# Kernel tuning notes

Hardware: AMD Instinct MI355X
Metric: run time of the kernel (lower is better)

The kernel has to match this reference:

```python
import jax, jax.numpy as jnp
import numpy as np

H, FFN, E, TOPK = 1024, 4096, 8, 2
B, S = 2, 1024


def setup_inputs() -> dict:
    key = jax.random.key(0)
    k1, k2, k3, k4 = jax.random.split(key, 4)
    s_h = 1.0 / np.sqrt(H).astype(np.float32)
    s_f = 1.0 / np.sqrt(FFN).astype(np.float32)
    return {
        "hidden_states": jax.random.normal(k1, (B, S, H), jnp.float32),
        "gate_w": jax.random.normal(k2, (E, H), jnp.float32) * s_h,       # router Linear(H->E), no bias
        "w13": jax.random.normal(k3, (E, 2 * FFN, H), jnp.float32) * s_h,  # fused [w1; w3] per expert
        "w2": jax.random.normal(k4, (E, H, FFN), jnp.float32) * s_f,       # down-proj per expert
        "top_k": TOPK,
    }


def reference(hidden_states, gate_w, w13, w2, top_k):
    b, s, h = hidden_states.shape
    x = hidden_states.reshape(-1, h)                       # [T, H]
    router_logits = x @ gate_w.T                           # [T, E]
    rw = jax.nn.softmax(router_logits.astype(jnp.float32), axis=1)
    rw, sel = jax.lax.top_k(rw, top_k)                     # [T, K] each
    rw = rw / rw.sum(axis=-1, keepdims=True)
    rw = rw.astype(x.dtype)
    e_tot = gate_w.shape[0]
    f = w2.shape[2]
    # combine[t, e] = sum_k rw[t, k] * (sel[t, k] == e)
    combine = jnp.sum((sel[..., None] == jnp.arange(e_tot)) * rw[..., None], axis=1)  # [T, E]
    out = jnp.zeros_like(x)
    for e in range(e_tot):  # static small loop over experts
        g = x @ w13[e, :f].T            # [T, F] gate proj
        u = x @ w13[e, f:].T            # [T, F] up proj
        y = (jax.nn.silu(g) * u) @ w2[e].T  # [T, H]
        out = out + combine[:, e:e + 1] * y
    return out.reshape(b, s, h), router_logits
```

## Files before the change

kernel.cpp:

```cpp
#include <hip/hip_runtime.h>
#include <hip/hip_bf16.h>
#include <math.h>

#define H     1024
#define FFN   4096
#define NE    8
#define TOK   2048
#define PAIRS (TOK*2)
#define BM    128
#define BK    32
#define ROWCAP (PAIRS + NE*BM)
#define MAXTILES (ROWCAP/BM)

typedef unsigned short u16;
typedef __attribute__((ext_vector_type(8))) __bf16 bf16x8;
typedef __attribute__((ext_vector_type(4))) float  f32x4;

__device__ __forceinline__ unsigned cvt2(float a, float b) {
    __hip_bfloat162 h = __float22bfloat162_rn(float2{a, b});
    unsigned u;
    __builtin_memcpy(&u, &h, 4);
    return u;
}

#define GLD16(gp, lp) __builtin_amdgcn_global_load_lds( \
    (const __attribute__((address_space(1))) void*)(gp), \
    (__attribute__((address_space(3))) void*)(lp), 16, 0, 0)


__global__ void k_init(int* counts) {
    if (threadIdx.x < NE) counts[threadIdx.x] = 0;
}

__global__ void k_router(const float* __restrict__ x, const float* __restrict__ gw,
                         float* __restrict__ logits, int* counts,
                         int* __restrict__ sel, int* __restrict__ posn, float* __restrict__ wgt) {
    int lane = threadIdx.x & 63;
    int t = blockIdx.x * 4 + (threadIdx.x >> 6);
    float p[NE];
#pragma unroll
    for (int e = 0; e < NE; e++) p[e] = 0.f;
    for (int j = 0; j < H / 64; j++) {
        int h = lane + j * 64;
        float xv = x[(size_t)t * H + h];
#pragma unroll
        for (int e = 0; e < NE; e++) p[e] = fmaf(xv, gw[e * H + h], p[e]);
    }
#pragma unroll
    for (int off = 32; off; off >>= 1)
#pragma unroll
        for (int e = 0; e < NE; e++) p[e] += __shfl_xor(p[e], off, 64);
    if (lane == 0) {
        float mx = p[0];
#pragma unroll
        for (int e = 1; e < NE; e++) mx = fmaxf(mx, p[e]);
        float pe[NE];
#pragma unroll
        for (int e = 0; e < NE; e++) pe[e] = __expf(p[e] - mx);
        int i0 = 0;
#pragma unroll
        for (int e = 1; e < NE; e++) if (pe[e] > pe[i0]) i0 = e;
        int i1 = (i0 == 0) ? 1 : 0;
#pragma unroll
        for (int e = 0; e < NE; e++) if (e != i1 && e != i0 && pe[e] > pe[i1]) i1 = e;
        float w0 = pe[i0] / (pe[i0] + pe[i1]);
#pragma unroll
        for (int e = 0; e < NE; e++) logits[(size_t)t * NE + e] = p[e];
        int p0 = atomicAdd(&counts[i0], 1);
        int p1 = atomicAdd(&counts[i1], 1);
        sel[2 * t] = i0;  posn[2 * t] = p0;  wgt[2 * t] = w0;
        sel[2 * t + 1] = i1;  posn[2 * t + 1] = p1;  wgt[2 * t + 1] = 1.f - w0;
    }
}

__global__ void k_prefix(const int* __restrict__ counts, int* __restrict__ base,
                         int* __restrict__ tile_e) {
    if (threadIdx.x == 0) {
        int b = 0, tb = 0;
        for (int e = 0; e < NE; e++) {
            base[e] = b;
            int nt = (counts[e] + BM - 1) / BM;
            for (int i = 0; i < nt; i++) tile_e[tb++] = e;
            b += nt * BM;
        }
        base[NE] = b;
        while (tb < MAXTILES) tile_e[tb++] = -1;
    }
}

__global__ void k_gather(const float4* __restrict__ x4, const int* __restrict__ sel,
                         const int* __restrict__ posn, const int* __restrict__ base,
                         u16* __restrict__ xg) {
    int p = blockIdx.x;
    int lane = threadIdx.x;
    int t = p >> 1;
    int row = base[sel[p]] + posn[p];
    int f2 = ((row >> 1) & 3) << 1;
#pragma unroll
    for (int i = 0; i < 4; i++) {
        int idx = i * 64 + lane;
        float4 v = x4[(size_t)t * (H / 4) + (idx ^ f2)];
        uint2 o = { cvt2(v.x, v.y), cvt2(v.z, v.w) };
        *(uint2*)&xg[(size_t)row * H + idx * 4] = o;
    }
}

__global__ __launch_bounds__(256) void k_gemm1(const u16* __restrict__ xg,
                                               const float* __restrict__ w13,
                                               u16* __restrict__ act,
                                               const int* __restrict__ tile_e) {
    int id = blockIdx.x;
    int xcd = id & 7;
    int j = id >> 3;
    int tile = j % MAXTILES;
    int n0i = xcd * 8 + j / MAXTILES;
    int e = tile_e[tile];
    if (e < 0) return;
    __shared__ u16 As[2][BM * BK];
    __shared__ u16 Bs[2][2][64 * (BK + 8)];

    int tid = threadIdx.x;
    int lane = tid & 63, wave = tid >> 6;
    int quad = lane >> 4, m16 = lane & 15;
    int wm = wave >> 1, wn = wave & 1;
    int row0 = tile * BM;
    int n0 = n0i * 64;
    const float* wb1 = w13 + ((size_t)e * 2 * FFN + n0) * H;
    const float* wb3 = w13 + ((size_t)e * 2 * FFN + FFN + n0) * H;

    f32x4 accg[4][2], accu[4][2];
#pragma unroll
    for (int mi = 0; mi < 4; mi++)
#pragma unroll
        for (int ni = 0; ni < 2; ni++) { accg[mi][ni] = {0.f,0.f,0.f,0.f}; accu[mi][ni] = {0.f,0.f,0.f,0.f}; }

    float4 v1[2], v3[2];
#pragma unroll
    for (int i = 0; i < 2; i++) {
        int chunk = i * 256 + tid;
        GLD16(xg + (size_t)(row0 + (chunk >> 2)) * H + (chunk & 3) * 8, As[0] + chunk * 8);
    }
#pragma unroll
    for (int i = 0; i < 2; i++) {
        int idx = i * 256 + tid;
        v1[i] = *(const float4*)(wb1 + (size_t)(idx >> 3) * H + (idx & 7) * 4);
        v3[i] = *(const float4*)(wb3 + (size_t)(idx >> 3) * H + (idx & 7) * 4);
    }
#pragma unroll
    for (int i = 0; i < 2; i++) {
        int idx = i * 256 + tid;
        int r = idx >> 3, c4 = idx & 7;
        uint2 o1 = { cvt2(v1[i].x, v1[i].y), cvt2(v1[i].z, v1[i].w) };
        uint2 o3 = { cvt2(v3[i].x, v3[i].y), cvt2(v3[i].z, v3[i].w) };
        *(uint2*)&Bs[0][0][r * (BK + 8) + c4 * 4] = o1;
        *(uint2*)&Bs[0][1][r * (BK + 8) + c4 * 4] = o3;
    }
    __syncthreads();

    int aslot = quad ^ ((m16 >> 1) & 3);
    for (int it = 0; it < H / BK; ++it) {
        int cur = it & 1, nxt = cur ^ 1;
        int kk = (it + 1) * BK;
        bool pf = kk < H;
        if (pf) {
#pragma unroll
            for (int i = 0; i < 2; i++) {
                int chunk = i * 256 + tid;
                GLD16(xg + (size_t)(row0 + (chunk >> 2)) * H + kk + (chunk & 3) * 8, As[nxt] + chunk * 8);
            }
#pragma unroll
            for (int i = 0; i < 2; i++) {
                int idx = i * 256 + tid;
                v1[i] = *(const float4*)(wb1 + (size_t)(idx >> 3) * H + kk + (idx & 7) * 4);
                v3[i] = *(const float4*)(wb3 + (size_t)(idx >> 3) * H + kk + (idx & 7) * 4);
            }
        }
        bf16x8 a[4], bg[2], bu[2];
#pragma unroll
        for (int mi = 0; mi < 4; mi++)
            a[mi] = *(const bf16x8*)&As[cur][(wm * 64 + mi * 16 + m16) * BK + aslot * 8];
#pragma unroll
        for (int ni = 0; ni < 2; ni++) {
            bg[ni] = *(const bf16x8*)&Bs[cur][0][(wn * 32 + ni * 16 + m16) * (BK + 8) + quad * 8];
            bu[ni] = *(const bf16x8*)&Bs[cur][1][(wn * 32 + ni * 16 + m16) * (BK + 8) + quad * 8];
        }
#pragma unroll
        for (int mi = 0; mi < 4; mi++)
#pragma unroll
            for (int ni = 0; ni < 2; ni++) {
                accg[mi][ni] = __builtin_amdgcn_mfma_f32_16x16x32_bf16(a[mi], bg[ni], accg[mi][ni], 0, 0, 0);
                accu[mi][ni] = __builtin_amdgcn_mfma_f32_16x16x32_bf16(a[mi], bu[ni], accu[mi][ni], 0, 0, 0);
            }
        __builtin_amdgcn_sched_barrier(0);
        if (pf) {
#pragma unroll
            for (int i = 0; i < 2; i++) {
                int idx = i * 256 + tid;
                int r = idx >> 3, c4 = idx & 7;
                uint2 o1 = { cvt2(v1[i].x, v1[i].y), cvt2(v1[i].z, v1[i].w) };
                uint2 o3 = { cvt2(v3[i].x, v3[i].y), cvt2(v3[i].z, v3[i].w) };
                *(uint2*)&Bs[nxt][0][r * (BK + 8) + c4 * 4] = o1;
                *(uint2*)&Bs[nxt][1][r * (BK + 8) + c4 * 4] = o3;
            }
        }
        __syncthreads();
    }
#pragma unroll
    for (int mi = 0; mi < 4; mi++)
#pragma unroll
        for (int ni = 0; ni < 2; ni++) {
            int gcol = n0 + wn * 32 + ni * 16 + m16;
            int grow = row0 + wm * 64 + mi * 16 + quad * 4;
#pragma unroll
            for (int r = 0; r < 4; r++) {
                float g = accg[mi][ni][r], u = accu[mi][ni][r];
                float hv = g * (1.f / (1.f + __expf(-g))) * u;
                int f = ((quad * 4 + r) >> 1) & 3;
                act[(size_t)(grow + r) * FFN + (gcol ^ (f << 3))] = (u16)(cvt2(hv, hv) & 0xffff);
            }
        }
}

__global__ __launch_bounds__(256) void k_gemm2(const u16* __restrict__ act,
                                               const float* __restrict__ w2,
                                               float* __restrict__ yc,
                                               const int* __restrict__ tile_e) {
    int id = blockIdx.x;
    int xcd = id & 7;
    int j = id >> 3;
    int tile = j % MAXTILES;
    int pz = xcd * 2 + j / MAXTILES;
    int e = tile_e[tile];
    if (e < 0) return;
    __shared__ u16 As[2][BM * BK];
    __shared__ u16 Bs[2][BM * (BK + 8)];

    int tid = threadIdx.x;
    int lane = tid & 63, wave = tid >> 6;
    int quad = lane >> 4, m16 = lane & 15;
    int wm = wave >> 1, wn = wave & 1;
    int row0 = tile * BM;
    int n0 = (pz >> 1) * 128;
    int z = pz & 1;
    int k0 = z * (FFN / 2);
    const float* wb = w2 + ((size_t)e * H + n0) * FFN;
    float* ycp = yc + (size_t)z * ROWCAP * H;

    f32x4 acc[4][4];
#pragma unroll
    for (int mi = 0; mi < 4; mi++)
#pragma unroll
        for (int ni = 0; ni < 4; ni++) acc[mi][ni] = {0.f,0.f,0.f,0.f};

    float4 v[4];
#pragma unroll
    for (int i = 0; i < 2; i++) {
        int chunk = i * 256 + tid;
        GLD16(act + (size_t)(row0 + (chunk >> 2)) * FFN + k0 + (chunk & 3) * 8, As[0] + chunk * 8);
    }
#pragma unroll
    for (int i = 0; i < 4; i++) {
        int idx = i * 256 + tid;
        v[i] = *(const float4*)(wb + (size_t)(idx >> 3) * FFN + k0 + (idx & 7) * 4);
    }
#pragma unroll
    for (int i = 0; i < 4; i++) {
        int idx = i * 256 + tid;
        int r = idx >> 3, c4 = idx & 7;
        uint2 o = { cvt2(v[i].x, v[i].y), cvt2(v[i].z, v[i].w) };
        *(uint2*)&Bs[0][r * (BK + 8) + c4 * 4] = o;
    }
    __syncthreads();

    int aslot = quad ^ ((m16 >> 1) & 3);
    const int NT = (FFN / 2) / BK;
    for (int it = 0; it < NT; ++it) {
        int cur = it & 1, nxt = cur ^ 1;
        int kk = k0 + (it + 1) * BK;
        bool pf = (it + 1) < NT;
        if (pf) {
#pragma unroll
            for (int i = 0; i < 2; i++) {
                int chunk = i * 256 + tid;
                GLD16(act + (size_t)(row0 + (chunk >> 2)) * FFN + kk + (chunk & 3) * 8, As[nxt] + chunk * 8);
            }
#pragma unroll
            for (int i = 0; i < 4; i++) {
                int idx = i * 256 + tid;
                v[i] = *(const float4*)(wb + (size_t)(idx >> 3) * FFN + kk + (idx & 7) * 4);
            }
        }
        bf16x8 a[4], b[4];
#pragma unroll
        for (int mi = 0; mi < 4; mi++)
            a[mi] = *(const bf16x8*)&As[cur][(wm * 64 + mi * 16 + m16) * BK + aslot * 8];
#pragma unroll
        for (int ni = 0; ni < 4; ni++)
            b[ni] = *(const bf16x8*)&Bs[cur][(wn * 64 + ni * 16 + m16) * (BK + 8) + quad * 8];
#pragma unroll
        for (int mi = 0; mi < 4; mi++)
#pragma unroll
            for (int ni = 0; ni < 4; ni++)
                acc[mi][ni] = __builtin_amdgcn_mfma_f32_16x16x32_bf16(a[mi], b[ni], acc[mi][ni], 0, 0, 0);
        __builtin_amdgcn_sched_barrier(0);
        if (pf) {
#pragma unroll
            for (int i = 0; i < 4; i++) {
                int idx = i * 256 + tid;
                int r = idx >> 3, c4 = idx & 7;
                uint2 o = { cvt2(v[i].x, v[i].y), cvt2(v[i].z, v[i].w) };
                *(uint2*)&Bs[nxt][r * (BK + 8) + c4 * 4] = o;
            }
        }
        __syncthreads();
    }
#pragma unroll
    for (int mi = 0; mi < 4; mi++)
#pragma unroll
        for (int ni = 0; ni < 4; ni++)
#pragma unroll
            for (int r = 0; r < 4; r++) {
                int grow = row0 + wm * 64 + mi * 16 + quad * 4 + r;
                int gcol = n0 + wn * 64 + ni * 16 + m16;
                ycp[(size_t)grow * H + gcol] = acc[mi][ni][r];
            }
}

__global__ void k_combine(const float4* __restrict__ yc4, const int* __restrict__ sel,
                          const int* __restrict__ posn, const int* __restrict__ base,
                          const float* __restrict__ wgt, float4* __restrict__ out4) {
    int t = blockIdx.x;
    int j = threadIdx.x;
    int r0 = base[sel[2 * t]] + posn[2 * t];
    int r1 = base[sel[2 * t + 1]] + posn[2 * t + 1];
    float w0 = wgt[2 * t], w1 = wgt[2 * t + 1];
    const size_t P = (size_t)ROWCAP * (H / 4);
    float4 a0 = yc4[(size_t)r0 * (H / 4) + j];
    float4 a1 = yc4[(size_t)r0 * (H / 4) + j + P];
    float4 b0 = yc4[(size_t)r1 * (H / 4) + j];
    float4 b1 = yc4[(size_t)r1 * (H / 4) + j + P];
    float4 o = { w0 * (a0.x + a1.x) + w1 * (b0.x + b1.x),
                 w0 * (a0.y + a1.y) + w1 * (b0.y + b1.y),
                 w0 * (a0.z + a1.z) + w1 * (b0.z + b1.z),
                 w0 * (a0.w + a1.w) + w1 * (b0.w + b1.w) };
    out4[(size_t)t * (H / 4) + j] = o;
}

extern "C" void kernel_launch(void* const* d_in, const int* in_sizes, int n_in,
                              void* d_out, int out_size, void* d_ws, size_t ws_size,
                              hipStream_t stream) {
    const float* x   = (const float*)d_in[0];
    const float* gw  = (const float*)d_in[1];
    const float* w13 = (const float*)d_in[2];
    const float* w2  = (const float*)d_in[3];
    float* out    = (float*)d_out;
    float* logits = out + (size_t)TOK * H;

    char* ws = (char*)d_ws;
    int*   counts = (int*)ws;
    int*   base   = (int*)(ws + 256);
    int*   tile_e = (int*)(ws + 512);
    int*   sel    = (int*)(ws + 1024);
    int*   posn   = (int*)(ws + 1024 + 4 * PAIRS);
    float* wgt    = (float*)(ws + 1024 + 8 * PAIRS);
    u16*   xg     = (u16*)(ws + 65536);
    u16*   act    = xg + (size_t)ROWCAP * H;
    float* yc     = (float*)(act + (size_t)ROWCAP * FFN);

    k_init<<<1, 64, 0, stream>>>(counts);
    k_router<<<TOK / 4, 256, 0, stream>>>(x, gw, logits, counts, sel, posn, wgt);
    k_prefix<<<1, 64, 0, stream>>>(counts, base, tile_e);
    k_gather<<<PAIRS, 64, 0, stream>>>((const float4*)x, sel, posn, base, xg);
    k_gemm1<<<dim3(MAXTILES * (FFN / 64)), 256, 0, stream>>>(xg, w13, act, tile_e);
    k_gemm2<<<dim3(MAXTILES * (H / 128) * 2), 256, 0, stream>>>(act, w2, yc, tile_e);
    k_combine<<<TOK, 256, 0, stream>>>((const float4*)yc, sel, posn, base, wgt, (float4*)out);
}
```

Measured before the change: 683.4 us.

## Deepen GEMM prefetch to distance two with triple-buffered A tiles

Both expert GEMM kernels now prefetch K-tiles two iterations ahead instead of one. The A tile gets three LDS buffers with a rotating index, and the fp32 weights get two register sets, with the loop unrolled by two to alternate them. The plain __syncthreads is replaced by a barrier that waits with s_waitcnt vmcnt(6), so the newest global loads can stay in flight across it. This aims to hide more global-load latency of the weight and activation streams, at the cost of extra LDS and registers that may lower occupancy.

```diff
diff --git a/kernel.cpp b/kernel.cpp
--- a/kernel.cpp
+++ b/kernel.cpp
@@ -11,6 +11,7 @@
 #define BK    32
 #define ROWCAP (PAIRS + NE*BM)
 #define MAXTILES (ROWCAP/BM)
+#define AT    (BM*BK)
 
 typedef unsigned short u16;
 typedef __attribute__((ext_vector_type(8))) __bf16 bf16x8;
@@ -27,6 +28,10 @@
     (const __attribute__((address_space(1))) void*)(gp), \
     (__attribute__((address_space(3))) void*)(lp), 16, 0, 0)
 
+#define PIPE_BARRIER() do { \
+    asm volatile("s_waitcnt vmcnt(6) lgkmcnt(0)" ::: "memory"); \
+    __builtin_amdgcn_s_barrier(); \
+} while (0)
 
 __global__ void k_init(int* counts) {
     if (threadIdx.x < NE) counts[threadIdx.x] = 0;
@@ -116,7 +121,7 @@
     int n0i = xcd * 8 + j / MAXTILES;
     int e = tile_e[tile];
     if (e < 0) return;
-    __shared__ u16 As[2][BM * BK];
+    __shared__ u16 As[3][AT];
     __shared__ u16 Bs[2][2][64 * (BK + 8)];
 
     int tid = threadIdx.x;
@@ -134,7 +139,11 @@
 #pragma unroll
         for (int ni = 0; ni < 2; ni++) { accg[mi][ni] = {0.f,0.f,0.f,0.f}; accu[mi][ni] = {0.f,0.f,0.f,0.f}; }
 
-    float4 v1[2], v3[2];
+    const int NT = H / BK;
+    float4 v1a[2], v3a[2], v1b[2], v3b[2];
+    int ia0 = 0, ia1 = 1, ia2 = 2;
+    int aslot = quad ^ ((m16 >> 1) & 3);
+
 #pragma unroll
     for (int i = 0; i < 2; i++) {
         int chunk = i * 256 + tid;
@@ -143,68 +152,87 @@
 #pragma unroll
     for (int i = 0; i < 2; i++) {
         int idx = i * 256 + tid;
-        v1[i] = *(const float4*)(wb1 + (size_t)(idx >> 3) * H + (idx & 7) * 4);
-        v3[i] = *(const float4*)(wb3 + (size_t)(idx >> 3) * H + (idx & 7) * 4);
+        v1a[i] = *(const float4*)(wb1 + (size_t)(idx >> 3) * H + (idx & 7) * 4);
+        v3a[i] = *(const float4*)(wb3 + (size_t)(idx >> 3) * H + (idx & 7) * 4);
+    }
+#pragma unroll
+    for (int i = 0; i < 2; i++) {
+        int chunk = i * 256 + tid;
+        GLD16(xg + (size_t)(row0 + (chunk >> 2)) * H + BK + (chunk & 3) * 8, As[1] + chunk * 8);
+    }
+#pragma unroll
+    for (int i = 0; i < 2; i++) {
+        int idx = i * 256 + tid;
+        v1b[i] = *(const float4*)(wb1 + (size_t)(idx >> 3) * H + BK + (idx & 7) * 4);
+        v3b[i] = *(const float4*)(wb3 + (size_t)(idx >> 3) * H + BK + (idx & 7) * 4);
     }
 #pragma unroll
     for (int i = 0; i < 2; i++) {
         int idx = i * 256 + tid;
         int r = idx >> 3, c4 = idx & 7;
-        uint2 o1 = { cvt2(v1[i].x, v1[i].y), cvt2(v1[i].z, v1[i].w) };
-        uint2 o3 = { cvt2(v3[i].x, v3[i].y), cvt2(v3[i].z, v3[i].w) };
+        uint2 o1 = { cvt2(v1a[i].x, v1a[i].y), cvt2(v1a[i].z, v1a[i].w) };
+        uint2 o3 = { cvt2(v3a[i].x, v3a[i].y), cvt2(v3a[i].z, v3a[i].w) };
         *(uint2*)&Bs[0][0][r * (BK + 8) + c4 * 4] = o1;
         *(uint2*)&Bs[0][1][r * (BK + 8) + c4 * 4] = o3;
     }
-    __syncthreads();
-
-    int aslot = quad ^ ((m16 >> 1) & 3);
-    for (int it = 0; it < H / BK; ++it) {
-        int cur = it & 1, nxt = cur ^ 1;
-        int kk = (it + 1) * BK;
-        bool pf = kk < H;
-        if (pf) {
-#pragma unroll
-            for (int i = 0; i < 2; i++) {
-                int chunk = i * 256 + tid;
-                GLD16(xg + (size_t)(row0 + (chunk >> 2)) * H + kk + (chunk & 3) * 8, As[nxt] + chunk * 8);
-            }
-#pragma unroll
-            for (int i = 0; i < 2; i++) {
-                int idx = i * 256 + tid;
-                v1[i] = *(const float4*)(wb1 + (size_t)(idx >> 3) * H + kk + (idx & 7) * 4);
-                v3[i] = *(const float4*)(wb3 + (size_t)(idx >> 3) * H + kk + (idx & 7) * 4);
-            }
-        }
-        bf16x8 a[4], bg[2], bu[2];
-#pragma unroll
-        for (int mi = 0; mi < 4; mi++)
-            a[mi] = *(const bf16x8*)&As[cur][(wm * 64 + mi * 16 + m16) * BK + aslot * 8];
-#pragma unroll
-        for (int ni = 0; ni < 2; ni++) {
-            bg[ni] = *(const bf16x8*)&Bs[cur][0][(wn * 32 + ni * 16 + m16) * (BK + 8) + quad * 8];
-            bu[ni] = *(const bf16x8*)&Bs[cur][1][(wn * 32 + ni * 16 + m16) * (BK + 8) + quad * 8];
-        }
-#pragma unroll
-        for (int mi = 0; mi < 4; mi++)
-#pragma unroll
-            for (int ni = 0; ni < 2; ni++) {
-                accg[mi][ni] = __builtin_amdgcn_mfma_f32_16x16x32_bf16(a[mi], bg[ni], accg[mi][ni], 0, 0, 0);
-                accu[mi][ni] = __builtin_amdgcn_mfma_f32_16x16x32_bf16(a[mi], bu[ni], accu[mi][ni], 0, 0, 0);
-            }
-        __builtin_amdgcn_sched_barrier(0);
-        if (pf) {
-#pragma unroll
-            for (int i = 0; i < 2; i++) {
-                int idx = i * 256 + tid;
-                int r = idx >> 3, c4 = idx & 7;
-                uint2 o1 = { cvt2(v1[i].x, v1[i].y), cvt2(v1[i].z, v1[i].w) };
-                uint2 o3 = { cvt2(v3[i].x, v3[i].y), cvt2(v3[i].z, v3[i].w) };
-                *(uint2*)&Bs[nxt][0][r * (BK + 8) + c4 * 4] = o1;
-                *(uint2*)&Bs[nxt][1][r * (BK + 8) + c4 * 4] = o3;
-            }
-        }
-        __syncthreads();
-    }
+    PIPE_BARRIER();
+
+#define G1_STEP(IT, V1L, V3L, V1C, V3C, BC, BN)                                             \
+    {                                                                                       \
+        int itp2 = (IT) + 2;                                                                \
+        if (itp2 < NT) {                                                                    \
+            int kk = itp2 * BK;                                                             \
+            _Pragma("unroll")                                                               \
+            for (int i = 0; i < 2; i++) {                                                   \
+                int chunk = i * 256 + tid;                                                  \
+                GLD16(xg + (size_t)(row0 + (chunk >> 2)) * H + kk + (chunk & 3) * 8,        \
+                      As[ia2] + chunk * 8);                                                 \
+            }                                                                               \
+            _Pragma("unroll")                                                               \
+            for (int i = 0; i < 2; i++) {                                                   \
+                int idx = i * 256 + tid;                                                    \
+                V1L[i] = *(const float4*)(wb1 + (size_t)(idx >> 3) * H + kk + (idx & 7) * 4);\
+                V3L[i] = *(const float4*)(wb3 + (size_t)(idx >> 3) * H + kk + (idx & 7) * 4);\
+            }                                                                               \
+        }                                                                                   \
+        bf16x8 a[4], bg[2], bu[2];                                                          \
+        _Pragma("unroll")                                                                   \
+        for (int mi = 0; mi < 4; mi++)                                                      \
+            a[mi] = *(const bf16x8*)&As[ia0][(wm * 64 + mi * 16 + m16) * BK + aslot * 8];   \
+        _Pragma("unroll")                                                                   \
+        for (int ni = 0; ni < 2; ni++) {                                                    \
+            bg[ni] = *(const bf16x8*)&Bs[BC][0][(wn * 32 + ni * 16 + m16) * (BK + 8) + quad * 8];\
+            bu[ni] = *(const bf16x8*)&Bs[BC][1][(wn * 32 + ni * 16 + m16) * (BK + 8) + quad * 8];\
+        }                                                                                   \
+        _Pragma("unroll")                                                                   \
+        for (int mi = 0; mi < 4; mi++)                                                      \
+            _Pragma("unroll")                                                               \
+            for (int ni = 0; ni < 2; ni++) {                                                \
+                accg[mi][ni] = __builtin_amdgcn_mfma_f32_16x16x32_bf16(a[mi], bg[ni], accg[mi][ni], 0, 0, 0);\
+                accu[mi][ni] = __builtin_amdgcn_mfma_f32_16x16x32_bf16(a[mi], bu[ni], accu[mi][ni], 0, 0, 0);\
+            }                                                                               \
+        __builtin_amdgcn_sched_barrier(0);                                                  \
+        if ((IT) + 1 < NT) {                                                                \
+            _Pragma("unroll")                                                               \
+            for (int i = 0; i < 2; i++) {                                                   \
+                int idx = i * 256 + tid;                                                    \
+                int r = idx >> 3, c4 = idx & 7;                                             \
+                uint2 o1 = { cvt2(V1C[i].x, V1C[i].y), cvt2(V1C[i].z, V1C[i].w) };          \
+                uint2 o3 = { cvt2(V3C[i].x, V3C[i].y), cvt2(V3C[i].z, V3C[i].w) };          \
+                *(uint2*)&Bs[BN][0][r * (BK + 8) + c4 * 4] = o1;                            \
+                *(uint2*)&Bs[BN][1][r * (BK + 8) + c4 * 4] = o3;                            \
+            }                                                                               \
+        }                                                                                   \
+        PIPE_BARRIER();                                                                     \
+        int rot = ia0; ia0 = ia1; ia1 = ia2; ia2 = rot;                                     \
+    }
+
+    for (int it = 0; it < NT; it += 2) {
+        G1_STEP(it,     v1a, v3a, v1b, v3b, 0, 1);
+        G1_STEP(it + 1, v1b, v3b, v1a, v3a, 1, 0);
+    }
+#undef G1_STEP
+
 #pragma unroll
     for (int mi = 0; mi < 4; mi++)
 #pragma unroll
@@ -232,7 +260,7 @@
     int pz = xcd * 2 + j / MAXTILES;
     int e = tile_e[tile];
     if (e < 0) return;
-    __shared__ u16 As[2][BM * BK];
+    __shared__ u16 As[3][AT];
     __shared__ u16 Bs[2][BM * (BK + 8)];
 
     int tid = threadIdx.x;
@@ -252,7 +280,11 @@
 #pragma unroll
         for (int ni = 0; ni < 4; ni++) acc[mi][ni] = {0.f,0.f,0.f,0.f};
 
-    float4 v[4];
+    const int NT = (FFN / 2) / BK;
+    float4 va[4], vb[4];
+    int ia0 = 0, ia1 = 1, ia2 = 2;
+    int aslot = quad ^ ((m16 >> 1) & 3);
+
 #pragma unroll
     for (int i = 0; i < 2; i++) {
         int chunk = i * 256 + tid;
@@ -261,59 +293,76 @@
 #pragma unroll
     for (int i = 0; i < 4; i++) {
         int idx = i * 256 + tid;
-        v[i] = *(const float4*)(wb + (size_t)(idx >> 3) * FFN + k0 + (idx & 7) * 4);
+        va[i] = *(const float4*)(wb + (size_t)(idx >> 3) * FFN + k0 + (idx & 7) * 4);
+    }
+#pragma unroll
+    for (int i = 0; i < 2; i++) {
+        int chunk = i * 256 + tid;
+        GLD16(act + (size_t)(row0 + (chunk >> 2)) * FFN + k0 + BK + (chunk & 3) * 8, As[1] + chunk * 8);
     }
 #pragma unroll
     for (int i = 0; i < 4; i++) {
         int idx = i * 256 + tid;
+        vb[i] = *(const float4*)(wb + (size_t)(idx >> 3) * FFN + k0 + BK + (idx & 7) * 4);
+    }
+#pragma unroll
+    for (int i = 0; i < 4; i++) {
+        int idx = i * 256 + tid;
         int r = idx >> 3, c4 = idx & 7;
-        uint2 o = { cvt2(v[i].x, v[i].y), cvt2(v[i].z, v[i].w) };
+        uint2 o = { cvt2(va[i].x, va[i].y), cvt2(va[i].z, va[i].w) };
         *(uint2*)&Bs[0][r * (BK + 8) + c4 * 4] = o;
     }
-    __syncthreads();
-
-    int aslot = quad ^ ((m16 >> 1) & 3);
-    const int NT = (FFN / 2) / BK;
-    for (int it = 0; it < NT; ++it) {
-        int cur = it & 1, nxt = cur ^ 1;
-        int kk = k0 + (it + 1) * BK;
-        bool pf = (it + 1) < NT;
-        if (pf) {
-#pragma unroll
-            for (int i = 0; i < 2; i++) {
-                int chunk = i * 256 + tid;
-                GLD16(act + (size_t)(row0 + (chunk >> 2)) * FFN + kk + (chunk & 3) * 8, As[nxt] + chunk * 8);
-            }
-#pragma unroll
-            for (int i = 0; i < 4; i++) {
-                int idx = i * 256 + tid;
-                v[i] = *(const float4*)(wb + (size_t)(idx >> 3) * FFN + kk + (idx & 7) * 4);
-            }
-        }
-        bf16x8 a[4], b[4];
-#pragma unroll
-        for (int mi = 0; mi < 4; mi++)
-            a[mi] = *(const bf16x8*)&As[cur][(wm * 64 + mi * 16 + m16) * BK + aslot * 8];
-#pragma unroll
-        for (int ni = 0; ni < 4; ni++)
-            b[ni] = *(const bf16x8*)&Bs[cur][(wn * 64 + ni * 16 + m16) * (BK + 8) + quad * 8];
-#pragma unroll
-        for (int mi = 0; mi < 4; mi++)
-#pragma unroll
-            for (int ni = 0; ni < 4; ni++)
-                acc[mi][ni] = __builtin_amdgcn_mfma_f32_16x16x32_bf16(a[mi], b[ni], acc[mi][ni], 0, 0, 0);
-        __builtin_amdgcn_sched_barrier(0);
-        if (pf) {
-#pragma unroll
-            for (int i = 0; i < 4; i++) {
-                int idx = i * 256 + tid;
-                int r = idx >> 3, c4 = idx & 7;
-                uint2 o = { cvt2(v[i].x, v[i].y), cvt2(v[i].z, v[i].w) };
-                *(uint2*)&Bs[nxt][r * (BK + 8) + c4 * 4] = o;
-            }
-        }
-        __syncthreads();
-    }
+    PIPE_BARRIER();
+
+#define G2_STEP(IT, VL, VC, BC, BN)                                                         \
+    {                                                                                       \
+        int itp2 = (IT) + 2;                                                                \
+        if (itp2 < NT) {                                                                    \
+            int kk = k0 + itp2 * BK;                                                        \
+            _Pragma("unroll")                                                               \
+            for (int i = 0; i < 2; i++) {                                                   \
+                int chunk = i * 256 + tid;                                                  \
+                GLD16(act + (size_t)(row0 + (chunk >> 2)) * FFN + kk + (chunk & 3) * 8,     \
+                      As[ia2] + chunk * 8);                                                 \
+            }                                                                               \
+            _Pragma("unroll")                                                               \
+            for (int i = 0; i < 4; i++) {                                                   \
+                int idx = i * 256 + tid;                                                    \
+                VL[i] = *(const float4*)(wb + (size_t)(idx >> 3) * FFN + kk + (idx & 7) * 4);\
+            }                                                                               \
+        }                                                                                   \
+        bf16x8 a[4], b[4];                                                                  \
+        _Pragma("unroll")                                                                   \
+        for (int mi = 0; mi < 4; mi++)                                                      \
+            a[mi] = *(const bf16x8*)&As[ia0][(wm * 64 + mi * 16 + m16) * BK + aslot * 8];   \
+        _Pragma("unroll")                                                                   \
+        for (int ni = 0; ni < 4; ni++)                                                      \
+            b[ni] = *(const bf16x8*)&Bs[BC][(wn * 64 + ni * 16 + m16) * (BK + 8) + quad * 8];\
+        _Pragma("unroll")                                                                   \
+        for (int mi = 0; mi < 4; mi++)                                                      \
+            _Pragma("unroll")                                                               \
+            for (int ni = 0; ni < 4; ni++)                                                  \
+                acc[mi][ni] = __builtin_amdgcn_mfma_f32_16x16x32_bf16(a[mi], b[ni], acc[mi][ni], 0, 0, 0);\
+        __builtin_amdgcn_sched_barrier(0);                                                  \
+        if ((IT) + 1 < NT) {                                                                \
+            _Pragma("unroll")                                                               \
+            for (int i = 0; i < 4; i++) {                                                   \
+                int idx = i * 256 + tid;                                                    \
+                int r = idx >> 3, c4 = idx & 7;                                             \
+                uint2 o = { cvt2(VC[i].x, VC[i].y), cvt2(VC[i].z, VC[i].w) };               \
+                *(uint2*)&Bs[BN][r * (BK + 8) + c4 * 4] = o;                                \
+            }                                                                               \
+        }                                                                                   \
+        PIPE_BARRIER();                                                                     \
+        int rot = ia0; ia0 = ia1; ia1 = ia2; ia2 = rot;                                     \
+    }
+
+    for (int it = 0; it < NT; it += 2) {
+        G2_STEP(it,     va, vb, 0, 1);
+        G2_STEP(it + 1, vb, va, 1, 0);
+    }
+#undef G2_STEP
+
 #pragma unroll
     for (int mi = 0; mi < 4; mi++)
 #pragma unroll
```

Result: slower. 786.6 us (+15.1%).

## Pre-convert expert weights to swizzled bf16 and use direct-to-LDS GEMMs

Applied to the files above, without the earlier changes.

Adds kernels that convert w13 and w2 from fp32 to bf16 in an XOR-swizzled layout in workspace on every call. New GEMM kernels then stream bf16 weights with global_load_lds straight into shared memory, replacing the fp32 weight loads and in-kernel conversion. The router prefix step is also parallelised across a wavefront. The conversion reads all weights, including tiles no token routes to, and writes a bf16 copy, so it adds memory traffic and needs a large workspace; without enough workspace the old fp32 path still runs.

```diff
diff --git a/kernel.cpp b/kernel.cpp
--- a/kernel.cpp
+++ b/kernel.cpp
@@ -32,6 +32,29 @@
     if (threadIdx.x < NE) counts[threadIdx.x] = 0;
 }
 
+__global__ void k_cvt13(const float4* __restrict__ w4, u16* __restrict__ wb) {
+    int t = threadIdx.x;
+#pragma unroll
+    for (int i = 0; i < 4; i++) {
+        int r = blockIdx.x * 4 + i;
+        int f2 = ((r >> 1) & 3) << 1;
+        float4 v = w4[(size_t)r * (H / 4) + t];
+        uint2 o = { cvt2(v.x, v.y), cvt2(v.z, v.w) };
+        *(uint2*)&wb[(size_t)r * H + ((t ^ f2) << 2)] = o;
+    }
+}
+__global__ void k_cvt2(const float4* __restrict__ w4, u16* __restrict__ wb) {
+    int r = blockIdx.x;
+    int f2 = ((r >> 1) & 3) << 1;
+#pragma unroll
+    for (int i = 0; i < 4; i++) {
+        int f = threadIdx.x + i * 256;
+        float4 v = w4[(size_t)r * (FFN / 4) + f];
+        uint2 o = { cvt2(v.x, v.y), cvt2(v.z, v.w) };
+        *(uint2*)&wb[(size_t)r * FFN + ((f ^ f2) << 2)] = o;
+    }
+}
+
 __global__ void k_router(const float* __restrict__ x, const float* __restrict__ gw,
                          float* __restrict__ logits, int* counts,
                          int* __restrict__ sel, int* __restrict__ posn, float* __restrict__ wgt) {
@@ -75,16 +98,25 @@
 
 __global__ void k_prefix(const int* __restrict__ counts, int* __restrict__ base,
                          int* __restrict__ tile_e) {
-    if (threadIdx.x == 0) {
-        int b = 0, tb = 0;
-        for (int e = 0; e < NE; e++) {
-            base[e] = b;
-            int nt = (counts[e] + BM - 1) / BM;
-            for (int i = 0; i < nt; i++) tile_e[tb++] = e;
-            b += nt * BM;
-        }
-        base[NE] = b;
-        while (tb < MAXTILES) tile_e[tb++] = -1;
+    int lane = threadIdx.x;
+    int cnt = (lane < NE) ? counts[lane] : 0;
+    int nt = (cnt + BM - 1) / BM;
+    int ntv[NE], tbv[NE];
+    int b = 0, tb = 0;
+#pragma unroll
+    for (int e = 0; e < NE; e++) {
+        int ne = __shfl(nt, e, 64);
+        ntv[e] = ne; tbv[e] = tb;
+        if (lane == e) base[e] = b;
+        tb += ne; b += ne * BM;
+    }
+    if (lane == 0) base[NE] = b;
+    if (lane < MAXTILES) {
+        int e = -1;
+#pragma unroll
+        for (int k = 0; k < NE; k++)
+            if (lane >= tbv[k] && lane < tbv[k] + ntv[k]) e = k;
+        tile_e[lane] = e;
     }
 }
 
@@ -105,10 +137,174 @@
     }
 }
 
-__global__ __launch_bounds__(256) void k_gemm1(const u16* __restrict__ xg,
-                                               const float* __restrict__ w13,
-                                               u16* __restrict__ act,
-                                               const int* __restrict__ tile_e) {
+__global__ __launch_bounds__(256) void k_gemm1b(const u16* __restrict__ xg,
+                                                const u16* __restrict__ w13b,
+                                                u16* __restrict__ act,
+                                                const int* __restrict__ tile_e) {
+    int id = blockIdx.x;
+    int xcd = id & 7;
+    int j = id >> 3;
+    int tile = j % MAXTILES;
+    int n0i = xcd * 8 + j / MAXTILES;
+    int e = tile_e[tile];
+    if (e < 0) return;
+    __shared__ u16 As[2][BM * BK];
+    __shared__ u16 B1s[2][64 * BK];
+    __shared__ u16 B3s[2][64 * BK];
+
+    int tid = threadIdx.x;
+    int lane = tid & 63, wave = tid >> 6;
+    int quad = lane >> 4, m16 = lane & 15;
+    int wm = wave >> 1, wn = wave & 1;
+    int row0 = tile * BM;
+    int n0 = n0i * 64;
+    const u16* wb1 = w13b + ((size_t)e * 2 * FFN + n0) * H;
+    const u16* wb3 = w13b + ((size_t)e * 2 * FFN + FFN + n0) * H;
+
+    f32x4 accg[4][2], accu[4][2];
+#pragma unroll
+    for (int mi = 0; mi < 4; mi++)
+#pragma unroll
+        for (int ni = 0; ni < 2; ni++) { accg[mi][ni] = {0.f,0.f,0.f,0.f}; accu[mi][ni] = {0.f,0.f,0.f,0.f}; }
+
+    int aslot = quad ^ ((m16 >> 1) & 3);
+    const int NT = H / BK;
+
+#define G1_STAGE(KK, BUF) {                                                              \
+        _Pragma("unroll")                                                                \
+        for (int i = 0; i < 2; i++) {                                                    \
+            int c = i * 256 + tid;                                                       \
+            GLD16(xg + (size_t)(row0 + (c >> 2)) * H + (KK) + (c & 3) * 8, As[BUF] + c * 8); \
+        }                                                                                \
+        GLD16(wb1 + (size_t)(tid >> 2) * H + (KK) + (tid & 3) * 8, B1s[BUF] + tid * 8);  \
+        GLD16(wb3 + (size_t)(tid >> 2) * H + (KK) + (tid & 3) * 8, B3s[BUF] + tid * 8);  \
+    }
+
+    G1_STAGE(0, 0);
+    __syncthreads();
+    for (int it = 0; it < NT; ++it) {
+        int cur = it & 1;
+        if (it + 1 < NT) G1_STAGE((it + 1) * BK, cur ^ 1);
+        bf16x8 a[4], bg[2], bu[2];
+#pragma unroll
+        for (int mi = 0; mi < 4; mi++)
+            a[mi] = *(const bf16x8*)&As[cur][(wm * 64 + mi * 16 + m16) * BK + aslot * 8];
+#pragma unroll
+        for (int ni = 0; ni < 2; ni++) {
+            bg[ni] = *(const bf16x8*)&B1s[cur][(wn * 32 + ni * 16 + m16) * BK + aslot * 8];
+            bu[ni] = *(const bf16x8*)&B3s[cur][(wn * 32 + ni * 16 + m16) * BK + aslot * 8];
+        }
+#pragma unroll
+        for (int mi = 0; mi < 4; mi++)
+#pragma unroll
+            for (int ni = 0; ni < 2; ni++) {
+                accg[mi][ni] = __builtin_amdgcn_mfma_f32_16x16x32_bf16(a[mi], bg[ni], accg[mi][ni], 0, 0, 0);
+                accu[mi][ni] = __builtin_amdgcn_mfma_f32_16x16x32_bf16(a[mi], bu[ni], accu[mi][ni], 0, 0, 0);
+            }
+        __syncthreads();
+    }
+#undef G1_STAGE
+
+#pragma unroll
+    for (int mi = 0; mi < 4; mi++)
+#pragma unroll
+        for (int ni = 0; ni < 2; ni++) {
+            int gcol = n0 + wn * 32 + ni * 16 + m16;
+            int grow = row0 + wm * 64 + mi * 16 + quad * 4;
+#pragma unroll
+            for (int r = 0; r < 4; r++) {
+                float g = accg[mi][ni][r], u = accu[mi][ni][r];
+                float hv = g * (1.f / (1.f + __expf(-g))) * u;
+                int f = ((quad * 4 + r) >> 1) & 3;
+                act[(size_t)(grow + r) * FFN + (gcol ^ (f << 3))] = (u16)(cvt2(hv, hv) & 0xffff);
+            }
+        }
+}
+
+__global__ __launch_bounds__(256) void k_gemm2b(const u16* __restrict__ act,
+                                                const u16* __restrict__ w2b,
+                                                float* __restrict__ yc,
+                                                const int* __restrict__ tile_e) {
+    int id = blockIdx.x;
+    int xcd = id & 7;
+    int j = id >> 3;
+    int tile = j % MAXTILES;
+    int pz = xcd * 2 + j / MAXTILES;
+    int e = tile_e[tile];
+    if (e < 0) return;
+    __shared__ u16 As[2][BM * BK];
+    __shared__ u16 Bs[2][BM * BK];
+
+    int tid = threadIdx.x;
+    int lane = tid & 63, wave = tid >> 6;
+    int quad = lane >> 4, m16 = lane & 15;
+    int wm = wave >> 1, wn = wave & 1;
+    int row0 = tile * BM;
+    int n0 = (pz >> 1) * 128;
+    int z = pz & 1;
+    int k0 = z * (FFN / 2);
+    const u16* wb = w2b + ((size_t)e * H + n0) * FFN;
+    float* ycp = yc + (size_t)z * ROWCAP * H;
+
+    f32x4 acc[4][4];
+#pragma unroll
+    for (int mi = 0; mi < 4; mi++)
+#pragma unroll
+        for (int ni = 0; ni < 4; ni++) acc[mi][ni] = {0.f,0.f,0.f,0.f};
+
+    int aslot = quad ^ ((m16 >> 1) & 3);
+    const int NT = (FFN / 2) / BK;
+
+#define G2_STAGE(KK, BUF) {                                                               \
+        _Pragma("unroll")                                                                 \
+        for (int i = 0; i < 2; i++) {                                                     \
+            int c = i * 256 + tid;                                                        \
+            GLD16(act + (size_t)(row0 + (c >> 2)) * FFN + (KK) + (c & 3) * 8, As[BUF] + c * 8); \
+        }                                                                                 \
+        _Pragma("unroll")                                                                 \
+        for (int i = 0; i < 2; i++) {                                                     \
+            int c = i * 256 + tid;                                                        \
+            GLD16(wb + (size_t)(c >> 2) * FFN + (KK) + (c & 3) * 8, Bs[BUF] + c * 8);     \
+        }                                                                                 \
+    }
+
+    G2_STAGE(k0, 0);
+    __syncthreads();
+    for (int it = 0; it < NT; ++it) {
+        int cur = it & 1;
+        if (it + 1 < NT) G2_STAGE(k0 + (it + 1) * BK, cur ^ 1);
+        bf16x8 a[4], b[4];
+#pragma unroll
+        for (int mi = 0; mi < 4; mi++)
+            a[mi] = *(const bf16x8*)&As[cur][(wm * 64 + mi * 16 + m16) * BK + aslot * 8];
+#pragma unroll
+        for (int ni = 0; ni < 4; ni++)
+            b[ni] = *(const bf16x8*)&Bs[cur][(wn * 64 + ni * 16 + m16) * BK + aslot * 8];
+#pragma unroll
+        for (int mi = 0; mi < 4; mi++)
+#pragma unroll
+            for (int ni = 0; ni < 4; ni++)
+                acc[mi][ni] = __builtin_amdgcn_mfma_f32_16x16x32_bf16(a[mi], b[ni], acc[mi][ni], 0, 0, 0);
+        __syncthreads();
+    }
+#undef G2_STAGE
+
+#pragma unroll
+    for (int mi = 0; mi < 4; mi++)
+#pragma unroll
+        for (int ni = 0; ni < 4; ni++)
+#pragma unroll
+            for (int r = 0; r < 4; r++) {
+                int grow = row0 + wm * 64 + mi * 16 + quad * 4 + r;
+                int gcol = n0 + wn * 64 + ni * 16 + m16;
+                ycp[(size_t)grow * H + gcol] = acc[mi][ni][r];
+            }
+}
+
+__global__ __launch_bounds__(256) void k_gemm1f(const u16* __restrict__ xg,
+                                                const float* __restrict__ w13,
+                                                u16* __restrict__ act,
+                                                const int* __restrict__ tile_e) {
     int id = blockIdx.x;
     int xcd = id & 7;
     int j = id >> 3;
@@ -221,10 +417,10 @@
         }
 }
 
-__global__ __launch_bounds__(256) void k_gemm2(const u16* __restrict__ act,
-                                               const float* __restrict__ w2,
-                                               float* __restrict__ yc,
-                                               const int* __restrict__ tile_e) {
+__global__ __launch_bounds__(256) void k_gemm2f(const u16* __restrict__ act,
+                                                const float* __restrict__ w2,
+                                                float* __restrict__ yc,
+                                                const int* __restrict__ tile_e) {
     int id = blockIdx.x;
     int xcd = id & 7;
     int j = id >> 3;
@@ -365,13 +561,30 @@
     float* wgt    = (float*)(ws + 1024 + 8 * PAIRS);
     u16*   xg     = (u16*)(ws + 65536);
     u16*   act    = xg + (size_t)ROWCAP * H;
-    float* yc     = (float*)(act + (size_t)ROWCAP * FFN);
+
+    const size_t W13B = (size_t)NE * 2 * FFN * H;
+    const size_t W2B  = (size_t)NE * H * FFN;
+    const size_t NEED = 65536 + (size_t)ROWCAP * H * 2 + (size_t)ROWCAP * FFN * 2
+                      + W13B * 2 + W2B * 2;
 
     k_init<<<1, 64, 0, stream>>>(counts);
     k_router<<<TOK / 4, 256, 0, stream>>>(x, gw, logits, counts, sel, posn, wgt);
     k_prefix<<<1, 64, 0, stream>>>(counts, base, tile_e);
     k_gather<<<PAIRS, 64, 0, stream>>>((const float4*)x, sel, posn, base, xg);
-    k_gemm1<<<dim3(MAXTILES * (FFN / 64)), 256, 0, stream>>>(xg, w13, act, tile_e);
-    k_gemm2<<<dim3(MAXTILES * (H / 128) * 2), 256, 0, stream>>>(act, w2, yc, tile_e);
-    k_combine<<<TOK, 256, 0, stream>>>((const float4*)yc, sel, posn, base, wgt, (float4*)out);
-}
+
+    if (ws_size >= NEED) {
+        u16* w13b = act + (size_t)ROWCAP * FFN;
+        u16* w2b  = w13b + W13B;
+        float* yc = (float*)w13b;
+        k_cvt13<<<NE * 2 * FFN / 4, 256, 0, stream>>>((const float4*)w13, w13b);
+        k_cvt2<<<NE * H, 256, 0, stream>>>((const float4*)w2, w2b);
+        k_gemm1b<<<dim3(MAXTILES * (FFN / 64)), 256, 0, stream>>>(xg, w13b, act, tile_e);
+        k_gemm2b<<<dim3(MAXTILES * (H / 128) * 2), 256, 0, stream>>>(act, w2b, yc, tile_e);
+        k_combine<<<TOK, 256, 0, stream>>>((const float4*)yc, sel, posn, base, wgt, (float4*)out);
+    } else {
+        float* yc = (float*)(act + (size_t)ROWCAP * FFN);
+        k_gemm1f<<<dim3(MAXTILES * (FFN / 64)), 256, 0, stream>>>(xg, w13, act, tile_e);
+        k_gemm2f<<<dim3(MAXTILES * (H / 128) * 2), 256, 0, stream>>>(act, w2, yc, tile_e);
+        k_combine<<<TOK, 256, 0, stream>>>((const float4*)yc, sel, posn, base, wgt, (float4*)out);
+    }
+}
```

Result: slower. 736.0 us (+7.7%).
